# Optimization experiments

Measured on AMD Instinct MI355X. Metric: run time of the kernel, lower is better.

## Reference

```python
import jax, jax.numpy as jnp
import numpy as np
from jax import lax

K = 3  # ksize (odd)


def _box_mean(x):
    """Edge-clipped k x k mean filter over the last two dims of [B,C,H,W].
    Equivalent to the torch Mean_Filter: sum over the window intersected
    with the image, divided by the actual number of in-bounds pixels."""
    H, W = x.shape[2], x.shape[3]
    sums = lax.reduce_window(x, 0.0, lax.add,
                             window_dimensions=(1, 1, K, K),
                             window_strides=(1, 1, 1, 1),
                             padding='SAME')
    counts = lax.reduce_window(jnp.ones((H, W), x.dtype), 0.0, lax.add,
                               window_dimensions=(K, K),
                               window_strides=(1, 1),
                               padding='SAME')  # [H,W] in-bounds counts
    return sums / counts[None, None, :, :]


def setup_inputs() -> dict:
    key = jax.random.key(0)
    k1, k2, k3 = jax.random.split(key, 3)
    B, C, H, W = 32, 64, 128, 128
    x = jax.random.normal(k1, (B, C, H, W), dtype=jnp.float32)
    # 1x1 conv weight [out_c, in_c] and bias, as in nn.Conv2d(64, 64, 1)
    conv_w = jax.random.normal(k2, (C, C), dtype=jnp.float32) * (1.0 / np.sqrt(C))
    conv_b = jax.random.normal(k3, (C,), dtype=jnp.float32) * 0.01
    return {"x": x, "conv_w": conv_w, "conv_b": conv_b}


def reference(x, conv_w, conv_b):
    # denoising_box forward: x + conv1x1(mean_filter(x))
    x_denoised = _box_mean(x)
    y = jnp.einsum('bchw,oc->bohw', x_denoised, conv_w) + conv_b[None, :, None, None]
    return x + y
```

## Files before the change

kernel.cpp:

```cpp
#include <hip/hip_runtime.h>

#define B_   32
#define C_   64
#define H_   128
#define W_   128
#define HW_  (H_ * W_)
#define CHW_ (C_ * HW_)
#define TH_  8

__global__ __launch_bounds__(256, 2) void denoise_fused(
    const float* __restrict__ x, const float* __restrict__ cw,
    const float* __restrict__ cb, float* __restrict__ out)
{
    __shared__ float tile[C_ * W_];
    __shared__ float Wt[C_ * C_];
    __shared__ float bias[C_];

    const int t  = threadIdx.x;
    const int b  = blockIdx.x >> 4;
    const int h0 = (blockIdx.x & 15) * TH_;

    for (int i = t; i < C_ * C_; i += 256) {
        int o = i >> 6, c = i & 63;
        Wt[c * 64 + o] = cw[i];
    }
    if (t < C_) bias[t] = cb[t];
    __syncthreads();

    const float* xb = x   + (size_t)b * CHW_;
    float*       ob = out + (size_t)b * CHW_;

    const int wt = t & 31;
    const int ot = t >> 5;

    for (int r = 0; r < TH_; ++r) {
        const int h = h0 + r;
        const bool hm = (h > 0), hp = (h < H_ - 1);

        const float4* rowc = (const float4*)(xb + h * W_);
        const float4* rowm = (const float4*)(xb + (h - 1) * W_);
        const float4* rowp = (const float4*)(xb + (h + 1) * W_);
        #pragma unroll
        for (int k = 0; k < 8; ++k) {
            int vi  = t + k * 256;
            int c   = vi >> 5;
            int f4  = vi & 31;
            int off = c * (HW_ / 4) + f4;
            float4 s = rowc[off];
            if (hm) { float4 a = rowm[off]; s.x += a.x; s.y += a.y; s.z += a.z; s.w += a.w; }
            if (hp) { float4 a = rowp[off]; s.x += a.x; s.y += a.y; s.z += a.z; s.w += a.w; }
            ((float4*)tile)[vi] = s;
        }
        __syncthreads();

        float4 xd[8];
        const float rv = 1.f + (hm ? 1.f : 0.f) + (hp ? 1.f : 0.f);
        const float i3 = 1.f / (rv * 3.f);
        const float i2 = 1.f / (rv * 2.f);
        #pragma unroll
        for (int k = 0; k < 8; ++k) {
            int vi = t + k * 256;
            int c  = vi >> 5;
            int w4 = (vi & 31) << 2;
            float4 v = ((const float4*)tile)[vi];
            float L = (w4 == 0)        ? 0.f : tile[c * W_ + w4 - 1];
            float R = (w4 == W_ - 4)   ? 0.f : tile[c * W_ + w4 + 4];
            float4 d;
            d.x = (L   + v.x + v.y) * ((w4 == 0)      ? i2 : i3);
            d.y = (v.x + v.y + v.z) * i3;
            d.z = (v.y + v.z + v.w) * i3;
            d.w = (v.z + v.w + R)   * ((w4 == W_ - 4) ? i2 : i3);
            xd[k] = d;
        }
        __syncthreads();
        #pragma unroll
        for (int k = 0; k < 8; ++k) ((float4*)tile)[t + k * 256] = xd[k];
        __syncthreads();

        float acc[8][4];
        #pragma unroll
        for (int oi = 0; oi < 8; ++oi) {
            float bv = bias[ot * 8 + oi];
            acc[oi][0] = bv; acc[oi][1] = bv; acc[oi][2] = bv; acc[oi][3] = bv;
        }
        #pragma unroll 4
        for (int c = 0; c < C_; ++c) {
            float4 xv = ((const float4*)tile)[c * 32 + wt];
            float4 wa = ((const float4*)Wt)[c * 16 + ot * 2];
            float4 wb = ((const float4*)Wt)[c * 16 + ot * 2 + 1];
            float w8[8] = { wa.x, wa.y, wa.z, wa.w, wb.x, wb.y, wb.z, wb.w };
            #pragma unroll
            for (int oi = 0; oi < 8; ++oi) {
                acc[oi][0] += w8[oi] * xv.x;
                acc[oi][1] += w8[oi] * xv.y;
                acc[oi][2] += w8[oi] * xv.z;
                acc[oi][3] += w8[oi] * xv.w;
            }
        }

        #pragma unroll
        for (int oi = 0; oi < 8; ++oi) {
            int o = ot * 8 + oi;
            const float4* xr = (const float4*)(xb + o * HW_ + h * W_);
            float4 v = xr[wt];
            float4 res;
            res.x = v.x + acc[oi][0];
            res.y = v.y + acc[oi][1];
            res.z = v.z + acc[oi][2];
            res.w = v.w + acc[oi][3];
            ((float4*)(ob + o * HW_ + h * W_))[wt] = res;
        }
        __syncthreads();
    }
}

extern "C" void kernel_launch(void* const* d_in, const int* in_sizes, int n_in,
                              void* d_out, int out_size, void* d_ws, size_t ws_size,
                              hipStream_t stream) {
    const float* x  = (const float*)d_in[0];
    const float* cw = (const float*)d_in[1];
    const float* cb = (const float*)d_in[2];
    float* out = (float*)d_out;
    dim3 grid(B_ * (H_ / TH_));
    dim3 block(256);
    hipLaunchKernelGGL(denoise_fused, grid, block, 0, stream, x, cw, cb, out);
}
```

Baseline: 317.8 us.

## Use wave shuffles for horizontal box sum and halve rows per block

Each wavefront now loads and sums the three vertical rows for its channels. It gets the left and right neighbours with __shfl_up/__shfl_down instead of staging partial sums in shared memory and reading them back. That removes one shared-memory pass and two barriers per row. Rows per block drop from 8 to 4, doubling the grid, and launch bounds request 3 blocks per SM. Bias moves to registers and the weight transpose goes through a padded shared buffer. Vertical halo rows are still re-read from global memory, and register pressure under the higher occupancy target could cause spills.

```diff
diff --git a/kernel.cpp b/kernel.cpp
--- a/kernel.cpp
+++ b/kernel.cpp
@@ -6,88 +6,77 @@
 #define W_   128
 #define HW_  (H_ * W_)
 #define CHW_ (C_ * HW_)
-#define TH_  8
+#define TH_  4
 
-__global__ __launch_bounds__(256, 2) void denoise_fused(
+__global__ __launch_bounds__(256, 3) void denoise_fused(
     const float* __restrict__ x, const float* __restrict__ cw,
     const float* __restrict__ cb, float* __restrict__ out)
 {
-    __shared__ float tile[C_ * W_];
+    __shared__ float xd[C_ * W_];
     __shared__ float Wt[C_ * C_];
-    __shared__ float bias[C_];
 
-    const int t  = threadIdx.x;
-    const int b  = blockIdx.x >> 4;
-    const int h0 = (blockIdx.x & 15) * TH_;
+    const int t    = threadIdx.x;
+    const int b    = blockIdx.x >> 5;
+    const int h0   = (blockIdx.x & 31) * TH_;
+    const int lane = t & 63;
+    const int wid  = t >> 6;
+    const int j    = lane & 31;
+    const int half = lane >> 5;
 
     for (int i = t; i < C_ * C_; i += 256) {
         int o = i >> 6, c = i & 63;
-        Wt[c * 64 + o] = cw[i];
+        xd[o * 65 + c] = cw[i];
     }
-    if (t < C_) bias[t] = cb[t];
+    __syncthreads();
+    for (int i = t; i < C_ * C_; i += 256) {
+        int c = i >> 6, o = i & 63;
+        Wt[i] = xd[o * 65 + c];
+    }
     __syncthreads();
 
     const float* xb = x   + (size_t)b * CHW_;
     float*       ob = out + (size_t)b * CHW_;
 
-    const int wt = t & 31;
-    const int ot = t >> 5;
+    const int o0 = wid * 16 + half * 8;
+    float bias[8];
+    #pragma unroll
+    for (int oi = 0; oi < 8; ++oi) bias[oi] = cb[o0 + oi];
 
     for (int r = 0; r < TH_; ++r) {
         const int h = h0 + r;
         const bool hm = (h > 0), hp = (h < H_ - 1);
-
-        const float4* rowc = (const float4*)(xb + h * W_);
-        const float4* rowm = (const float4*)(xb + (h - 1) * W_);
-        const float4* rowp = (const float4*)(xb + (h + 1) * W_);
-        #pragma unroll
-        for (int k = 0; k < 8; ++k) {
-            int vi  = t + k * 256;
-            int c   = vi >> 5;
-            int f4  = vi & 31;
-            int off = c * (HW_ / 4) + f4;
-            float4 s = rowc[off];
-            if (hm) { float4 a = rowm[off]; s.x += a.x; s.y += a.y; s.z += a.z; s.w += a.w; }
-            if (hp) { float4 a = rowp[off]; s.x += a.x; s.y += a.y; s.z += a.z; s.w += a.w; }
-            ((float4*)tile)[vi] = s;
-        }
-        __syncthreads();
-
-        float4 xd[8];
         const float rv = 1.f + (hm ? 1.f : 0.f) + (hp ? 1.f : 0.f);
         const float i3 = 1.f / (rv * 3.f);
         const float i2 = 1.f / (rv * 2.f);
+
         #pragma unroll
-        for (int k = 0; k < 8; ++k) {
-            int vi = t + k * 256;
-            int c  = vi >> 5;
-            int w4 = (vi & 31) << 2;
-            float4 v = ((const float4*)tile)[vi];
-            float L = (w4 == 0)        ? 0.f : tile[c * W_ + w4 - 1];
-            float R = (w4 == W_ - 4)   ? 0.f : tile[c * W_ + w4 + 4];
+        for (int p = 0; p < 8; ++p) {
+            const int c = p * 8 + wid * 2 + half;
+            const float* rc = xb + c * HW_ + h * W_;
+            float4 v = ((const float4*)rc)[j];
+            if (hm) { float4 a = ((const float4*)(rc - W_))[j]; v.x += a.x; v.y += a.y; v.z += a.z; v.w += a.w; }
+            if (hp) { float4 a = ((const float4*)(rc + W_))[j]; v.x += a.x; v.y += a.y; v.z += a.z; v.w += a.w; }
+            float L = __shfl_up(v.w, 1);
+            float R = __shfl_down(v.x, 1);
             float4 d;
-            d.x = (L   + v.x + v.y) * ((w4 == 0)      ? i2 : i3);
+            d.x = (j == 0)  ? (v.x + v.y) * i2 : (L + v.x + v.y) * i3;
             d.y = (v.x + v.y + v.z) * i3;
             d.z = (v.y + v.z + v.w) * i3;
-            d.w = (v.z + v.w + R)   * ((w4 == W_ - 4) ? i2 : i3);
-            xd[k] = d;
+            d.w = (j == 31) ? (v.z + v.w) * i2 : (v.z + v.w + R) * i3;
+            ((float4*)xd)[c * 32 + j] = d;
         }
-        __syncthreads();
-        #pragma unroll
-        for (int k = 0; k < 8; ++k) ((float4*)tile)[t + k * 256] = xd[k];
         __syncthreads();
 
         float acc[8][4];
         #pragma unroll
-        for (int oi = 0; oi < 8; ++oi) {
-            float bv = bias[ot * 8 + oi];
-            acc[oi][0] = bv; acc[oi][1] = bv; acc[oi][2] = bv; acc[oi][3] = bv;
-        }
+        for (int oi = 0; oi < 8; ++oi)
+            acc[oi][0] = acc[oi][1] = acc[oi][2] = acc[oi][3] = 0.f;
+
         #pragma unroll 4
         for (int c = 0; c < C_; ++c) {
-            float4 xv = ((const float4*)tile)[c * 32 + wt];
-            float4 wa = ((const float4*)Wt)[c * 16 + ot * 2];
-            float4 wb = ((const float4*)Wt)[c * 16 + ot * 2 + 1];
+            float4 xv = ((const float4*)xd)[c * 32 + j];
+            float4 wa = *(const float4*)&Wt[c * 64 + o0];
+            float4 wb = *(const float4*)&Wt[c * 64 + o0 + 4];
             float w8[8] = { wa.x, wa.y, wa.z, wa.w, wb.x, wb.y, wb.z, wb.w };
             #pragma unroll
             for (int oi = 0; oi < 8; ++oi) {
@@ -100,15 +89,14 @@
 
         #pragma unroll
         for (int oi = 0; oi < 8; ++oi) {
-            int o = ot * 8 + oi;
-            const float4* xr = (const float4*)(xb + o * HW_ + h * W_);
-            float4 v = xr[wt];
+            const int o = o0 + oi;
+            float4 xr = ((const float4*)(xb + o * HW_ + h * W_))[j];
             float4 res;
-            res.x = v.x + acc[oi][0];
-            res.y = v.y + acc[oi][1];
-            res.z = v.z + acc[oi][2];
-            res.w = v.w + acc[oi][3];
-            ((float4*)(ob + o * HW_ + h * W_))[wt] = res;
+            res.x = xr.x + acc[oi][0] + bias[oi];
+            res.y = xr.y + acc[oi][1] + bias[oi];
+            res.z = xr.z + acc[oi][2] + bias[oi];
+            res.w = xr.w + acc[oi][3] + bias[oi];
+            ((float4*)(ob + o * HW_ + h * W_))[j] = res;
         }
         __syncthreads();
     }
```

After: 313.3 us. Within noise of the previous version (-1.4%).
